# Kernel tuning notes

Hardware: AMD Instinct MI355X
Metric: run time of the kernel (lower is better)

The kernel has to match this reference:

```python
import jax, jax.numpy as jnp
import numpy as np

B, NDOCK, DCELL, C, H, W, HD = 65536, 3, 25, 32, 8, 8, 16


def setup_inputs() -> dict:
    key = jax.random.key(0)
    ks = jax.random.split(key, 10)
    s_q = 1.0 / np.sqrt(DCELL)
    s_kv = 1.0 / np.sqrt(C)
    s_o = 1.0 / np.sqrt(HD)
    return {
        "dock_masks": jax.random.uniform(ks[0], (B, NDOCK, DCELL), dtype=jnp.float32),
        "grid_feat": jax.random.normal(ks[1], (B, C, H, W), dtype=jnp.float32),
        "Wq": jax.random.uniform(ks[2], (HD, DCELL), jnp.float32, -s_q, s_q),
        "bq": jax.random.uniform(ks[3], (HD,), jnp.float32, -s_q, s_q),
        "Wk": jax.random.uniform(ks[4], (HD, C), jnp.float32, -s_kv, s_kv),  # conv1x1 kernel squeezed
        "bk": jax.random.uniform(ks[5], (HD,), jnp.float32, -s_kv, s_kv),
        "Wv": jax.random.uniform(ks[6], (HD, C), jnp.float32, -s_kv, s_kv),
        "bv": jax.random.uniform(ks[7], (HD,), jnp.float32, -s_kv, s_kv),
        "Wo": jax.random.uniform(ks[8], (HD, HD), jnp.float32, -s_o, s_o),
        "bo": jax.random.uniform(ks[9], (HD,), jnp.float32, -s_o, s_o),
    }


def reference(dock_masks, grid_feat, Wq, bq, Wk, bk, Wv, bv, Wo, bo):
    b = dock_masks.shape[0]
    hd = Wq.shape[0]
    # Q: [B, 3, hd]
    q = jnp.einsum("bnc,dc->bnd", dock_masks, Wq) + bq
    # K, V via 1x1 conv == channel matmul: [B, hd, H*W]
    g = grid_feat.reshape(b, grid_feat.shape[1], -1)  # [B, C, HW]
    k = jnp.einsum("bcs,dc->bds", g, Wk) + bk[None, :, None]
    v = jnp.einsum("bcs,dc->bds", g, Wv) + bv[None, :, None]
    # attention: [B, 3, HW]
    attn = jax.nn.softmax(jnp.einsum("bnd,bds->bns", q, k) / jnp.sqrt(jnp.float32(hd)), axis=-1)
    # context: [B, 3, hd]
    ctx = jnp.einsum("bns,bds->bnd", attn, v)
    out = jnp.einsum("bnd,ed->bne", ctx, Wo) + bo
    return out.reshape(b, -1)
```

## Files before the change

kernel.cpp:

```cpp
#include <hip/hip_runtime.h>


#define NW 4
#define GTS 66

__global__ void precompute_kernel(const float* __restrict__ Wq, const float* __restrict__ bq,
                                  const float* __restrict__ Wk, const float* __restrict__ Wv,
                                  const float* __restrict__ bv, const float* __restrict__ Wo,
                                  const float* __restrict__ bo, float* __restrict__ ws)
{
    const float K = 0.25f * 1.44269504088896f;
    const int t = threadIdx.x;
    for (int i = t; i < 800; i += 256) {
        int j = i >> 5, c = i & 31;
        float s = 0.f;
        #pragma unroll
        for (int d = 0; d < 16; ++d) s += Wq[d * 25 + j] * Wk[d * 32 + c];
        ws[i] = s * K;
    }
    if (t < 32) {
        float s = 0.f;
        #pragma unroll
        for (int d = 0; d < 16; ++d) s += bq[d] * Wk[d * 32 + t];
        ws[800 + t] = s * K;
    }
    for (int i = t; i < 512; i += 256) {
        int e = i >> 5, c = i & 31;
        float s = 0.f;
        #pragma unroll
        for (int d = 0; d < 16; ++d) s += Wo[e * 16 + d] * Wv[d * 32 + c];
        ws[832 + i] = s;
    }
    if (t < 16) {
        float s = bo[t];
        #pragma unroll
        for (int d = 0; d < 16; ++d) s += Wo[t * 16 + d] * bv[d];
        ws[1344 + t] = s;
    }
}

__device__ __forceinline__ float rl(float v, int srclane) {
    return __int_as_float(__builtin_amdgcn_readlane(__float_as_int(v), srclane));
}

__global__ __launch_bounds__(256, 4) void dock_attn_kernel(
    const float* __restrict__ dock,
    const float* __restrict__ grid,
    const float* __restrict__ ws,
    float* __restrict__ out,
    int b_total)
{
    __shared__ __align__(16) float AL[NW][96];
    __shared__ __align__(16) float attnL[NW][3 * 64];
    __shared__ __align__(16) float gT[NW][32 * GTS];
    __shared__ __align__(16) float zL[NW][96];

    const int tid = threadIdx.x;
    const int w = tid >> 6, lane = tid & 63;
    const int b = blockIdx.x * NW + w;
    if (b >= b_total) return;

    const float* Mg  = ws;
    const float* bkt = ws + 800;
    const float* Ug  = ws + 832;
    const float* c0  = ws + 1344;

    float d0 = dock[(size_t)b * 75 + lane];
    float d1 = (lane < 11) ? dock[(size_t)b * 75 + 64 + lane] : 0.f;
    const float* gp = grid + (size_t)b * 2048 + lane;
    float g[32];
    #pragma unroll
    for (int c = 0; c < 32; ++c) g[c] = gp[c * 64];

    if (lane < 32) {
        float bi = bkt[lane];
        float a0 = bi, a1 = bi, a2 = bi;
        #pragma unroll
        for (int j = 0; j < 25; ++j) {
            float m = Mg[j * 32 + lane];
            float q0 = rl(d0, j);
            float q1 = rl(d0, 25 + j);
            float q2 = (50 + j < 64) ? rl(d0, 50 + j) : rl(d1, 50 + j - 64);
            a0 = fmaf(q0, m, a0);
            a1 = fmaf(q1, m, a1);
            a2 = fmaf(q2, m, a2);
        }
        AL[w][lane] = a0; AL[w][32 + lane] = a1; AL[w][64 + lane] = a2;
    }

    float sc0 = 0.f, sc1 = 0.f, sc2 = 0.f;
    {
        const float4* A4 = (const float4*)&AL[w][0];
        #pragma unroll
        for (int q = 0; q < 8; ++q) {
            float4 a = A4[q], bb = A4[8 + q], cc = A4[16 + q];
            float g0 = g[4 * q], g1 = g[4 * q + 1], g2 = g[4 * q + 2], g3 = g[4 * q + 3];
            sc0 = fmaf(a.x, g0, fmaf(a.y, g1, fmaf(a.z, g2, fmaf(a.w, g3, sc0))));
            sc1 = fmaf(bb.x, g0, fmaf(bb.y, g1, fmaf(bb.z, g2, fmaf(bb.w, g3, sc1))));
            sc2 = fmaf(cc.x, g0, fmaf(cc.y, g1, fmaf(cc.z, g2, fmaf(cc.w, g3, sc2))));
        }
    }

    #pragma unroll
    for (int c = 0; c < 32; ++c) gT[w][c * GTS + lane] = g[c];

    float at0, at1, at2;
    {
        float m0 = sc0, m1 = sc1, m2 = sc2;
        #pragma unroll
        for (int off = 1; off < 64; off <<= 1) {
            m0 = fmaxf(m0, __shfl_xor(m0, off));
            m1 = fmaxf(m1, __shfl_xor(m1, off));
            m2 = fmaxf(m2, __shfl_xor(m2, off));
        }
        at0 = exp2f(sc0 - m0); at1 = exp2f(sc1 - m1); at2 = exp2f(sc2 - m2);
        float s0 = at0, s1 = at1, s2 = at2;
        #pragma unroll
        for (int off = 1; off < 64; off <<= 1) {
            s0 += __shfl_xor(s0, off);
            s1 += __shfl_xor(s1, off);
            s2 += __shfl_xor(s2, off);
        }
        at0 *= __builtin_amdgcn_rcpf(s0);
        at1 *= __builtin_amdgcn_rcpf(s1);
        at2 *= __builtin_amdgcn_rcpf(s2);
    }
    attnL[w][lane] = at0; attnL[w][64 + lane] = at1; attnL[w][128 + lane] = at2;

    {
        const int n = lane >> 5, c = lane & 31;
        const float2* ar = (const float2*)&attnL[w][n * 64];
        const float2* gr = (const float2*)&gT[w][c * GTS];
        float ax = 0.f, ay = 0.f;
        #pragma unroll
        for (int j = 0; j < 32; ++j) {
            float2 a = ar[j], gg = gr[j];
            ax = fmaf(a.x, gg.x, ax);
            ay = fmaf(a.y, gg.y, ay);
        }
        zL[w][n * 32 + c] = ax + ay;
    }
    if (lane < 32) {
        const float2* ar = (const float2*)&attnL[w][128];
        const float2* gr = (const float2*)&gT[w][lane * GTS];
        float ax = 0.f, ay = 0.f;
        #pragma unroll
        for (int j = 0; j < 32; ++j) {
            float2 a = ar[j], gg = gr[j];
            ax = fmaf(a.x, gg.x, ax);
            ay = fmaf(a.y, gg.y, ay);
        }
        zL[w][64 + lane] = ax + ay;
    }

    if (lane < 48) {
        const int n = lane >> 4, e = lane & 15;
        const float4* Ur = (const float4*)(Ug + e * 32);
        const float4* zr = (const float4*)&zL[w][n * 32];
        float acc0 = c0[e], acc1 = 0.f, acc2 = 0.f, acc3 = 0.f;
        #pragma unroll
        for (int q = 0; q < 8; ++q) {
            float4 u = Ur[q], z = zr[q];
            acc0 = fmaf(u.x, z.x, acc0);
            acc1 = fmaf(u.y, z.y, acc1);
            acc2 = fmaf(u.z, z.z, acc2);
            acc3 = fmaf(u.w, z.w, acc3);
        }
        out[(size_t)b * 48 + lane] = (acc0 + acc1) + (acc2 + acc3);
    }
}

extern "C" void kernel_launch(void* const* d_in, const int* in_sizes, int n_in,
                              void* d_out, int out_size, void* d_ws, size_t ws_size,
                              hipStream_t stream) {
    const float* dock = (const float*)d_in[0];
    const float* grid = (const float*)d_in[1];
    const float* Wq   = (const float*)d_in[2];
    const float* bq   = (const float*)d_in[3];
    const float* Wk   = (const float*)d_in[4];
    const float* Wv   = (const float*)d_in[6];
    const float* bv   = (const float*)d_in[7];
    const float* Wo   = (const float*)d_in[8];
    const float* bo   = (const float*)d_in[9];
    float* out = (float*)d_out;
    float* ws  = (float*)d_ws;

    precompute_kernel<<<1, 256, 0, stream>>>(Wq, bq, Wk, Wv, bv, Wo, bo, ws);

    const int b_total = in_sizes[0] / 75;
    const int blocks = (b_total + NW - 1) / NW;
    dock_attn_kernel<<<blocks, 256, 0, stream>>>(dock, grid, ws, out, b_total);
}
```

Before: 712.6 us.

## Load grid directly into swizzled LDS and drop softmax max reduction

The grid tile is now copied global-to-LDS with global_load_lds 16-byte transfers into an XOR-swizzled layout instead of going through registers, so score and context reads pull from LDS. The softmax no longer subtracts the row max or does cross-lane sum shuffles. Normalization is deferred: unnormalized exp weights feed the context dot products, row sums are computed by three extra lanes, and the reciprocal is applied at the output projection. Skipping the max subtraction risks overflow for large scores. The Mg weights are also hoisted into registers before the grid loads.

```diff
diff --git a/kernel.cpp b/kernel.cpp
--- a/kernel.cpp
+++ b/kernel.cpp
@@ -2,7 +2,6 @@
 
 
 #define NW 4
-#define GTS 66
 
 __global__ void precompute_kernel(const float* __restrict__ Wq, const float* __restrict__ bq,
                                   const float* __restrict__ Wk, const float* __restrict__ Wv,
@@ -43,6 +42,12 @@
     return __int_as_float(__builtin_amdgcn_readlane(__float_as_int(v), srclane));
 }
 
+__device__ __forceinline__ void gload_lds16(const float* src, float* dst_lds) {
+    __builtin_amdgcn_global_load_lds(
+        (const __attribute__((address_space(1))) void*)src,
+        (__attribute__((address_space(3))) void*)dst_lds, 16, 0, 0);
+}
+
 __global__ __launch_bounds__(256, 4) void dock_attn_kernel(
     const float* __restrict__ dock,
     const float* __restrict__ grid,
@@ -50,10 +55,10 @@
     float* __restrict__ out,
     int b_total)
 {
+    __shared__ __align__(16) float gT[NW][2048];
     __shared__ __align__(16) float AL[NW][96];
-    __shared__ __align__(16) float attnL[NW][3 * 64];
-    __shared__ __align__(16) float gT[NW][32 * GTS];
-    __shared__ __align__(16) float zL[NW][96];
+    __shared__ __align__(16) float attnL[NW][192];
+    __shared__ __align__(16) float zL[NW][104];
 
     const int tid = threadIdx.x;
     const int w = tid >> 6, lane = tid & 63;
@@ -65,19 +70,34 @@
     const float* Ug  = ws + 832;
     const float* c0  = ws + 1344;
 
+    float mreg[25];
+    float bi = 0.f;
+    if (lane < 32) {
+        #pragma unroll
+        for (int j = 0; j < 25; ++j) mreg[j] = Mg[j * 32 + lane];
+        bi = bkt[lane];
+    }
     float d0 = dock[(size_t)b * 75 + lane];
     float d1 = (lane < 11) ? dock[(size_t)b * 75 + 64 + lane] : 0.f;
-    const float* gp = grid + (size_t)b * 2048 + lane;
-    float g[32];
-    #pragma unroll
-    for (int c = 0; c < 32; ++c) g[c] = gp[c * 64];
+
+    asm volatile("" ::: "memory");
+
+    {
+        const float* gb = grid + (size_t)b * 2048;
+        const int h = lane >> 4, q = lane & 15;
+        #pragma unroll
+        for (int i = 0; i < 8; ++i) {
+            const int c = 4 * i + h;
+            const int s4 = q ^ (c & 15);
+            gload_lds16(gb + c * 64 + 4 * s4, &gT[w][i * 256]);
+        }
+    }
 
     if (lane < 32) {
-        float bi = bkt[lane];
         float a0 = bi, a1 = bi, a2 = bi;
         #pragma unroll
         for (int j = 0; j < 25; ++j) {
-            float m = Mg[j * 32 + lane];
+            float m = mreg[j];
             float q0 = rl(d0, j);
             float q1 = rl(d0, 25 + j);
             float q2 = (50 + j < 64) ? rl(d0, 50 + j) : rl(d1, 50 + j - 64);
@@ -88,85 +108,87 @@
         AL[w][lane] = a0; AL[w][32 + lane] = a1; AL[w][64 + lane] = a2;
     }
 
+    asm volatile("s_waitcnt vmcnt(0)" ::: "memory");
+
     float sc0 = 0.f, sc1 = 0.f, sc2 = 0.f;
     {
+        const float* gTw = &gT[w][0];
         const float4* A4 = (const float4*)&AL[w][0];
         #pragma unroll
-        for (int q = 0; q < 8; ++q) {
-            float4 a = A4[q], bb = A4[8 + q], cc = A4[16 + q];
-            float g0 = g[4 * q], g1 = g[4 * q + 1], g2 = g[4 * q + 2], g3 = g[4 * q + 3];
+        for (int qq = 0; qq < 8; ++qq) {
+            float4 a = A4[qq], bb = A4[8 + qq], cc = A4[16 + qq];
+            const int c = 4 * qq;
+            float g0 = gTw[((c + 0) << 6) + (lane ^ (((c + 0) & 15) << 2))];
+            float g1 = gTw[((c + 1) << 6) + (lane ^ (((c + 1) & 15) << 2))];
+            float g2 = gTw[((c + 2) << 6) + (lane ^ (((c + 2) & 15) << 2))];
+            float g3 = gTw[((c + 3) << 6) + (lane ^ (((c + 3) & 15) << 2))];
             sc0 = fmaf(a.x, g0, fmaf(a.y, g1, fmaf(a.z, g2, fmaf(a.w, g3, sc0))));
             sc1 = fmaf(bb.x, g0, fmaf(bb.y, g1, fmaf(bb.z, g2, fmaf(bb.w, g3, sc1))));
             sc2 = fmaf(cc.x, g0, fmaf(cc.y, g1, fmaf(cc.z, g2, fmaf(cc.w, g3, sc2))));
         }
     }
 
-    #pragma unroll
-    for (int c = 0; c < 32; ++c) gT[w][c * GTS + lane] = g[c];
-
-    float at0, at1, at2;
+    attnL[w][lane]       = exp2f(sc0);
+    attnL[w][64 + lane]  = exp2f(sc1);
+    attnL[w][128 + lane] = exp2f(sc2);
+
     {
-        float m0 = sc0, m1 = sc1, m2 = sc2;
-        #pragma unroll
-        for (int off = 1; off < 64; off <<= 1) {
-            m0 = fmaxf(m0, __shfl_xor(m0, off));
-            m1 = fmaxf(m1, __shfl_xor(m1, off));
-            m2 = fmaxf(m2, __shfl_xor(m2, off));
-        }
-        at0 = exp2f(sc0 - m0); at1 = exp2f(sc1 - m1); at2 = exp2f(sc2 - m2);
-        float s0 = at0, s1 = at1, s2 = at2;
-        #pragma unroll
-        for (int off = 1; off < 64; off <<= 1) {
-            s0 += __shfl_xor(s0, off);
-            s1 += __shfl_xor(s1, off);
-            s2 += __shfl_xor(s2, off);
-        }
-        at0 *= __builtin_amdgcn_rcpf(s0);
-        at1 *= __builtin_amdgcn_rcpf(s1);
-        at2 *= __builtin_amdgcn_rcpf(s2);
-    }
-    attnL[w][lane] = at0; attnL[w][64 + lane] = at1; attnL[w][128 + lane] = at2;
-
-    {
-        const int n = lane >> 5, c = lane & 31;
-        const float2* ar = (const float2*)&attnL[w][n * 64];
-        const float2* gr = (const float2*)&gT[w][c * GTS];
-        float ax = 0.f, ay = 0.f;
-        #pragma unroll
-        for (int j = 0; j < 32; ++j) {
-            float2 a = ar[j], gg = gr[j];
+        const int n = lane >> 5, c = lane & 31, cx = c & 15;
+        const float4* ar = (const float4*)&attnL[w][n * 64];
+        const float* grow = &gT[w][c << 6];
+        float ax = 0.f, ay = 0.f, az = 0.f, aw = 0.f;
+        #pragma unroll
+        for (int j = 0; j < 16; ++j) {
+            float4 a  = ar[j];
+            float4 gg = *(const float4*)&grow[(j ^ cx) << 2];
             ax = fmaf(a.x, gg.x, ax);
             ay = fmaf(a.y, gg.y, ay);
-        }
-        zL[w][n * 32 + c] = ax + ay;
+            az = fmaf(a.z, gg.z, az);
+            aw = fmaf(a.w, gg.w, aw);
+        }
+        zL[w][n * 32 + c] = (ax + ay) + (az + aw);
     }
     if (lane < 32) {
-        const float2* ar = (const float2*)&attnL[w][128];
-        const float2* gr = (const float2*)&gT[w][lane * GTS];
-        float ax = 0.f, ay = 0.f;
-        #pragma unroll
-        for (int j = 0; j < 32; ++j) {
-            float2 a = ar[j], gg = gr[j];
+        const int cx = lane & 15;
+        const float4* ar = (const float4*)&attnL[w][128];
+        const float* grow = &gT[w][lane << 6];
+        float ax = 0.f, ay = 0.f, az = 0.f, aw = 0.f;
+        #pragma unroll
+        for (int j = 0; j < 16; ++j) {
+            float4 a  = ar[j];
+            float4 gg = *(const float4*)&grow[(j ^ cx) << 2];
             ax = fmaf(a.x, gg.x, ax);
             ay = fmaf(a.y, gg.y, ay);
-        }
-        zL[w][64 + lane] = ax + ay;
+            az = fmaf(a.z, gg.z, az);
+            aw = fmaf(a.w, gg.w, aw);
+        }
+        zL[w][64 + lane] = (ax + ay) + (az + aw);
+    } else if (lane < 35) {
+        const float4* ar = (const float4*)&attnL[w][(lane - 32) * 64];
+        float s0 = 0.f, s1 = 0.f, s2 = 0.f, s3 = 0.f;
+        #pragma unroll
+        for (int j = 0; j < 16; ++j) {
+            float4 a = ar[j];
+            s0 += a.x; s1 += a.y; s2 += a.z; s3 += a.w;
+        }
+        zL[w][96 + (lane - 32)] = (s0 + s1) + (s2 + s3);
     }
 
     if (lane < 48) {
         const int n = lane >> 4, e = lane & 15;
         const float4* Ur = (const float4*)(Ug + e * 32);
         const float4* zr = (const float4*)&zL[w][n * 32];
-        float acc0 = c0[e], acc1 = 0.f, acc2 = 0.f, acc3 = 0.f;
-        #pragma unroll
-        for (int q = 0; q < 8; ++q) {
-            float4 u = Ur[q], z = zr[q];
+        float dinv = __builtin_amdgcn_rcpf(zL[w][96 + n]);
+        float acc0 = 0.f, acc1 = 0.f, acc2 = 0.f, acc3 = 0.f;
+        #pragma unroll
+        for (int qq = 0; qq < 8; ++qq) {
+            float4 u = Ur[qq], z = zr[qq];
             acc0 = fmaf(u.x, z.x, acc0);
             acc1 = fmaf(u.y, z.y, acc1);
             acc2 = fmaf(u.z, z.z, acc2);
             acc3 = fmaf(u.w, z.w, acc3);
         }
-        out[(size_t)b * 48 + lane] = (acc0 + acc1) + (acc2 + acc3);
+        out[(size_t)b * 48 + lane] = fmaf((acc0 + acc1) + (acc2 + acc3), dinv, c0[e]);
     }
 }
 
```

Measured after the change: 715.2 us. No clear change (+0.4%).
